# Optimization experiments

Hardware: AMD Instinct MI355X
Metric: run time of the kernel (lower is better)

The kernel has to match this reference:

```python
import jax, jax.numpy as jnp
import numpy as np

BLOCK = 512  # circulant block size

def block_circulant_matmul(x, w):
    """Block-circulant linear layer (CirCNN-style), no bias.
    x: (..., p*BLOCK); w: (q, p, BLOCK) -> out: (..., q*BLOCK).
    Each (q,p) block is a circulant matrix applied via FFT (circular conv).
    """
    q, p, b = w.shape
    xb = x.reshape(x.shape[:-1] + (p, b))            # (..., p, b)
    Xf = jnp.fft.rfft(xb, axis=-1)                    # (..., p, b//2+1) complex
    Wf = jnp.fft.rfft(w, axis=-1)                     # (q, p, b//2+1)
    Yf = jnp.einsum('...pf,qpf->...qf', Xf, Wf)       # sum over input blocks
    y = jnp.fft.irfft(Yf, n=b, axis=-1)               # (..., q, b)
    return y.reshape(x.shape[:-1] + (q * b,))

def setup_inputs() -> dict:
    key = jax.random.key(0)
    k1, k2, k3, k4 = jax.random.split(key, 4)
    d_model, d_ff, b = 2048, 5632, BLOCK
    p_in, q_ff = d_model // b, d_ff // b              # 4, 11
    scale = 1.0 / np.sqrt(d_model)
    x = jax.random.normal(k1, (4, 4096, d_model), dtype=jnp.float32)
    w_gate = jax.random.normal(k2, (q_ff, p_in, b), dtype=jnp.float32) * scale
    w_up   = jax.random.normal(k3, (q_ff, p_in, b), dtype=jnp.float32) * scale
    w_down = jax.random.normal(k4, (p_in, q_ff, b), dtype=jnp.float32) * (1.0 / np.sqrt(d_ff))
    return {"x": x, "w_gate": w_gate, "w_up": w_up, "w_down": w_down}

def reference(x, w_gate, w_up, w_down):
    # SwiGLU: down( SiLU(gate(x)) * up(x) ); dropout=0 -> identity
    gate = jax.nn.silu(block_circulant_matmul(x, w_gate))
    up = block_circulant_matmul(x, w_up)
    return block_circulant_matmul(gate * up, w_down)
```

## Files before the change

### kernel.cpp

```cpp
#include <hip/hip_runtime.h>
#include <math.h>


__device__ __forceinline__ int swz(int n) { return n ^ ((n >> 3) & 15); }

struct Tw { float t0r[7], t0i[7], t1r[7], t1i[7]; };

__device__ __forceinline__ void make_tw(int l, Tw& T)
{
    float c0, s0;
    __sincosf(-6.283185307179586f * (float)l * (1.0f/512.0f), &s0, &c0);
    float pr = c0, pi = s0;
    T.t0r[0] = pr; T.t0i[0] = pi;
#pragma unroll
    for (int m = 1; m < 7; ++m) {
        float nr = pr*c0 - pi*s0, ni = pr*s0 + pi*c0;
        pr = nr; pi = ni;
        T.t0r[m] = pr; T.t0i[m] = pi;
    }
    float c1, s1;
    __sincosf(-6.283185307179586f * (float)(l >> 3) * (1.0f/64.0f), &s1, &c1);
    pr = c1; pi = s1;
    T.t1r[0] = pr; T.t1i[0] = pi;
#pragma unroll
    for (int m = 1; m < 7; ++m) {
        float nr = pr*c1 - pi*s1, ni = pr*s1 + pi*c1;
        pr = nr; pi = ni;
        T.t1r[m] = pr; T.t1i[m] = pi;
    }
}

template<bool INV>
__device__ __forceinline__ void dft8(float xr[8], float xi[8])
{
    const float C = 0.70710678118654752f;
    float tr[4], ti[4], ur[4], ui[4];
#pragma unroll
    for (int q = 0; q < 4; ++q) {
        tr[q] = xr[q] + xr[q+4];  ti[q] = xi[q] + xi[q+4];
        ur[q] = xr[q] - xr[q+4];  ui[q] = xi[q] - xi[q+4];
    }
    {
        float xx = ur[1], yy = ui[1];
        if (!INV) { ur[1] = C*(xx+yy); ui[1] = C*(yy-xx); }
        else      { ur[1] = C*(xx-yy); ui[1] = C*(xx+yy); }
    }
    {
        float xx = ur[2], yy = ui[2];
        if (!INV) { ur[2] = yy;  ui[2] = -xx; }
        else      { ur[2] = -yy; ui[2] = xx; }
    }
    {
        float xx = ur[3], yy = ui[3];
        if (!INV) { ur[3] = C*(yy-xx);  ui[3] = -C*(xx+yy); }
        else      { ur[3] = -C*(xx+yy); ui[3] = C*(xx-yy); }
    }
    {
        float s0r=tr[0]+tr[2], s0i=ti[0]+ti[2];
        float d0r=tr[0]-tr[2], d0i=ti[0]-ti[2];
        float s1r=tr[1]+tr[3], s1i=ti[1]+ti[3];
        float e1r=tr[1]-tr[3], e1i=ti[1]-ti[3];
        float d1r, d1i;
        if (!INV) { d1r = e1i;  d1i = -e1r; } else { d1r = -e1i; d1i = e1r; }
        xr[0]=s0r+s1r; xi[0]=s0i+s1i;
        xr[2]=d0r+d1r; xi[2]=d0i+d1i;
        xr[4]=s0r-s1r; xi[4]=s0i-s1i;
        xr[6]=d0r-d1r; xi[6]=d0i-d1i;
    }
    {
        float s0r=ur[0]+ur[2], s0i=ui[0]+ui[2];
        float d0r=ur[0]-ur[2], d0i=ui[0]-ui[2];
        float s1r=ur[1]+ur[3], s1i=ui[1]+ui[3];
        float e1r=ur[1]-ur[3], e1i=ui[1]-ui[3];
        float d1r, d1i;
        if (!INV) { d1r = e1i;  d1i = -e1r; } else { d1r = -e1i; d1i = e1r; }
        xr[1]=s0r+s1r; xi[1]=s0i+s1i;
        xr[3]=d0r+d1r; xi[3]=d0i+d1i;
        xr[5]=s0r-s1r; xi[5]=s0i-s1i;
        xr[7]=d0r-d1r; xi[7]=d0i-d1i;
    }
}

template<bool INV>
__device__ __forceinline__ void twiddle7(float xr[8], float xi[8],
                                         const float* tr, const float* ti)
{
#pragma unroll
    for (int m = 1; m < 8; ++m) {
        float wr = tr[m-1], wi = INV ? -ti[m-1] : ti[m-1];
        float nr = xr[m]*wr - xi[m]*wi, ni = xr[m]*wi + xi[m]*wr;
        xr[m]=nr; xi[m]=ni;
    }
}

template<bool INV>
__device__ __forceinline__ void fft512_r8(float2* wk, int l, const Tw& T)
{
    float xr[8], xi[8];
#pragma unroll
    for (int q = 0; q < 8; ++q) { float2 v = wk[swz(l + 64*q)]; xr[q]=v.x; xi[q]=v.y; }
    dft8<INV>(xr, xi);
    twiddle7<INV>(xr, xi, T.t0r, T.t0i);
#pragma unroll
    for (int m = 0; m < 8; ++m) wk[swz(8*l + m)] = make_float2(xr[m], xi[m]);
#pragma unroll
    for (int q = 0; q < 8; ++q) { float2 v = wk[swz(l + 64*q)]; xr[q]=v.x; xi[q]=v.y; }
    dft8<INV>(xr, xi);
    twiddle7<INV>(xr, xi, T.t1r, T.t1i);
    {
        const int base = 64*(l>>3) + (l&7);
#pragma unroll
        for (int m = 0; m < 8; ++m) wk[swz(base + 8*m)] = make_float2(xr[m], xi[m]);
    }
#pragma unroll
    for (int q = 0; q < 8; ++q) { float2 v = wk[swz(l + 64*q)]; xr[q]=v.x; xi[q]=v.y; }
    dft8<INV>(xr, xi);
#pragma unroll
    for (int m = 0; m < 8; ++m) wk[swz(l + 64*m)] = make_float2(xr[m], xi[m]);
}

template<bool INV>
__device__ __forceinline__ void fft512_r8_head(float2* wk, int l, const Tw& T,
                                               float xr[8], float xi[8])
{
#pragma unroll
    for (int q = 0; q < 8; ++q) { float2 v = wk[swz(l + 64*q)]; xr[q]=v.x; xi[q]=v.y; }
    dft8<INV>(xr, xi);
    twiddle7<INV>(xr, xi, T.t0r, T.t0i);
#pragma unroll
    for (int m = 0; m < 8; ++m) wk[swz(8*l + m)] = make_float2(xr[m], xi[m]);
#pragma unroll
    for (int q = 0; q < 8; ++q) { float2 v = wk[swz(l + 64*q)]; xr[q]=v.x; xi[q]=v.y; }
    dft8<INV>(xr, xi);
    twiddle7<INV>(xr, xi, T.t1r, T.t1i);
    {
        const int base = 64*(l>>3) + (l&7);
#pragma unroll
        for (int m = 0; m < 8; ++m) wk[swz(base + 8*m)] = make_float2(xr[m], xi[m]);
    }
#pragma unroll
    for (int q = 0; q < 8; ++q) { float2 v = wk[swz(l + 64*q)]; xr[q]=v.x; xi[q]=v.y; }
    dft8<INV>(xr, xi);
}

template<bool INV>
__device__ __forceinline__ void fft512_r8_tail(float2* wk, int l, const Tw& T,
                                               float xr[8], float xi[8])
{
    dft8<INV>(xr, xi);
    twiddle7<INV>(xr, xi, T.t0r, T.t0i);
#pragma unroll
    for (int m = 0; m < 8; ++m) wk[swz(8*l + m)] = make_float2(xr[m], xi[m]);
#pragma unroll
    for (int q = 0; q < 8; ++q) { float2 v = wk[swz(l + 64*q)]; xr[q]=v.x; xi[q]=v.y; }
    dft8<INV>(xr, xi);
    twiddle7<INV>(xr, xi, T.t1r, T.t1i);
    {
        const int base = 64*(l>>3) + (l&7);
#pragma unroll
        for (int m = 0; m < 8; ++m) wk[swz(base + 8*m)] = make_float2(xr[m], xi[m]);
    }
#pragma unroll
    for (int q = 0; q < 8; ++q) { float2 v = wk[swz(l + 64*q)]; xr[q]=v.x; xi[q]=v.y; }
    dft8<INV>(xr, xi);
#pragma unroll
    for (int m = 0; m < 8; ++m) wk[swz(l + 64*m)] = make_float2(xr[m], xi[m]);
}

__global__ __launch_bounds__(64) void wf_prep(const float* __restrict__ wg,
                                              const float* __restrict__ wu,
                                              const float* __restrict__ wd,
                                              float2* __restrict__ wsp)
{
    __shared__ float2 wk[512];
    const int t = threadIdx.x;
    Tw T; make_tw(t, T);
    const int b = blockIdx.x;
    const float* src = (b < 44) ? (wg + (size_t)b * 512)
                     : (b < 88) ? (wu + (size_t)(b - 44) * 512)
                                : (wd + (size_t)(b - 88) * 512);
    float2* dst = wsp + (size_t)b * 257;

#pragma unroll
    for (int i = 0; i < 8; ++i) { int n = t + 64*i; wk[swz(n)] = make_float2(src[n], 0.f); }
    fft512_r8<false>(wk, t, T);
    const float sc = 1.0f / 512.0f;
#pragma unroll
    for (int i = 0; i < 5; ++i) {
        int k = t + 64*i;
        if (k <= 256) { float2 z = wk[swz(k)]; dst[k] = make_float2(sc*z.x, sc*z.y); }
    }
}

__global__ __launch_bounds__(256) void bcffn(const float* __restrict__ x,
                                             const float2* __restrict__ wsp,
                                             float* __restrict__ out)
{
    __shared__ float2 sWork[4 * 512];
    __shared__ float2 sXf[4][257];
    __shared__ float2 sHf[11][257];

    const int tid = threadIdx.x;
    const int t = tid & 63, w = tid >> 6;
    const size_t row = blockIdx.x;

    Tw T; make_tw(t, T);

    const float2* Wg = wsp;
    const float2* Wu = wsp + 44 * 257;
    const float2* Wd = wsp + 88 * 257;

    float2* wk = sWork + (w << 9);

    if (w < 2) {
        const float4* xa = (const float4*)(x + row * 2048 + (size_t)(2*w)   * 512);
        const float4* xb = (const float4*)(x + row * 2048 + (size_t)(2*w+1) * 512);
#pragma unroll
        for (int u = 0; u < 2; ++u) {
            int e = t + 64*u;
            float4 a = xa[e], b = xb[e];
            int n = 4*e;
            wk[swz(n+0)] = make_float2(a.x, b.x);
            wk[swz(n+1)] = make_float2(a.y, b.y);
            wk[swz(n+2)] = make_float2(a.z, b.z);
            wk[swz(n+3)] = make_float2(a.w, b.w);
        }
        fft512_r8<false>(wk, t, T);
#pragma unroll
        for (int u = 0; u < 5; ++u) {
            int k = t + 64*u;
            if (k <= 256) {
                float2 z = wk[swz(k)], m = wk[swz((512 - k) & 511)];
                sXf[2*w][k]   = make_float2(0.5f*(z.x + m.x), 0.5f*(z.y - m.y));
                sXf[2*w+1][k] = make_float2(0.5f*(z.y + m.y), 0.5f*(m.x - z.x));
            }
        }
    }
    __syncthreads();

    auto einsum_gu = [&](int q) {
#pragma unroll
        for (int u = 0; u < 5; ++u) {
            int k = t + 64*u;
            if (k <= 256) {
                float gr=0.f, gi=0.f, ur_=0.f, ui_=0.f;
#pragma unroll
                for (int p = 0; p < 4; ++p) {
                    float2 X = sXf[p][k];
                    float2 a = Wg[(q*4 + p)*257 + k];
                    float2 b = Wu[(q*4 + p)*257 + k];
                    gr  += X.x*a.x - X.y*a.y;  gi  += X.x*a.y + X.y*a.x;
                    ur_ += X.x*b.x - X.y*b.y;  ui_ += X.x*b.y + X.y*b.x;
                }
                wk[swz(k)] = make_float2(gr - ui_, gi + ur_);
                if (k != 0 && k != 256)
                    wk[swz(512 - k)] = make_float2(gr + ui_, ur_ - gi);
            }
        }
    };

    {
        const int qa = w, qb = w + 4;
        float har[8];
        float xr[8], xi[8];

        einsum_gu(qa);
        fft512_r8_head<true>(wk, t, T, xr, xi);
#pragma unroll
        for (int u = 0; u < 8; ++u)
            har[u] = xr[u] * xi[u] / (1.f + __expf(-xr[u]));

        einsum_gu(qb);
        fft512_r8_head<true>(wk, t, T, xr, xi);
#pragma unroll
        for (int u = 0; u < 8; ++u) {
            float hb = xr[u] * xi[u] / (1.f + __expf(-xr[u]));
            xr[u] = har[u];  xi[u] = hb;
        }
        fft512_r8_tail<false>(wk, t, T, xr, xi);
#pragma unroll
        for (int u = 0; u < 5; ++u) {
            int k = t + 64*u;
            if (k <= 256) {
                float2 z = wk[swz(k)], m = wk[swz((512 - k) & 511)];
                sHf[qa][k] = make_float2(0.5f*(z.x + m.x), 0.5f*(z.y - m.y));
                sHf[qb][k] = make_float2(0.5f*(z.y + m.y), 0.5f*(m.x - z.x));
            }
        }

        if (w < 3) {
            const int qc = w + 8;
            einsum_gu(qc);
            fft512_r8_head<true>(wk, t, T, xr, xi);
#pragma unroll
            for (int u = 0; u < 8; ++u) {
                xr[u] = xr[u] * xi[u] / (1.f + __expf(-xr[u]));
                xi[u] = 0.f;
            }
            fft512_r8_tail<false>(wk, t, T, xr, xi);
#pragma unroll
            for (int u = 0; u < 5; ++u) {
                int k = t + 64*u;
                if (k <= 256) sHf[qc][k] = wk[swz(k)];
            }
        }
    }
    __syncthreads();

    float Zr[5] = {0.f,0.f,0.f,0.f,0.f};
    float Zi[5] = {0.f,0.f,0.f,0.f,0.f};
#pragma unroll
    for (int u = 0; u < 5; ++u) {
        int k = t + 64*u;
        if (k <= 256) {
            float zr = 0.f, zi = 0.f;
#pragma unroll
            for (int q = 0; q < 11; ++q) {
                float2 H = sHf[q][k];
                float2 d = Wd[(w*11 + q)*257 + k];
                zr += H.x*d.x - H.y*d.y;
                zi += H.x*d.y + H.y*d.x;
            }
            Zr[u] = zr; Zi[u] = zi;
        }
    }
    if (w >= 2) {
#pragma unroll
        for (int u = 0; u < 5; ++u) {
            int k = t + 64*u;
            if (k <= 256) sXf[w-2][k] = make_float2(Zr[u], Zi[u]);
        }
    }
    __syncthreads();
    if (w < 2) {
#pragma unroll
        for (int u = 0; u < 5; ++u) {
            int k = t + 64*u;
            if (k <= 256) {
                float2 zb = sXf[w][k];
                wk[swz(k)] = make_float2(Zr[u] - zb.y, Zi[u] + zb.x);
                if (k != 0 && k != 256)
                    wk[swz(512 - k)] = make_float2(Zr[u] + zb.y, zb.x - Zi[u]);
            }
        }
        fft512_r8<true>(wk, t, T);
        float4* oa = (float4*)(out + row * 2048 + (size_t)w       * 512);
        float4* ob = (float4*)(out + row * 2048 + (size_t)(w + 2) * 512);
#pragma unroll
        for (int u = 0; u < 2; ++u) {
            int e = t + 64*u, n = 4*e;
            float2 v0 = wk[swz(n)],   v1 = wk[swz(n+1)];
            float2 v2 = wk[swz(n+2)], v3 = wk[swz(n+3)];
            oa[e] = make_float4(v0.x, v1.x, v2.x, v3.x);
            ob[e] = make_float4(v0.y, v1.y, v2.y, v3.y);
        }
    }
}

extern "C" void kernel_launch(void* const* d_in, const int* in_sizes, int n_in,
                              void* d_out, int out_size, void* d_ws, size_t ws_size,
                              hipStream_t stream)
{
    (void)n_in; (void)out_size; (void)ws_size;
    const float* x  = (const float*)d_in[0];
    const float* wg = (const float*)d_in[1];
    const float* wu = (const float*)d_in[2];
    const float* wd = (const float*)d_in[3];
    float2* wsp = (float2*)d_ws;
    float*  out = (float*)d_out;

    const int rows = in_sizes[0] / 2048;

    wf_prep<<<132, 64, 0, stream>>>(wg, wu, wd, wsp);
    bcffn<<<rows, 256, 0, stream>>>(x, wsp, out);
}
```

Before: 554.1 us.

## Process two rows per block with 8 waves and store spectra in half precision

Each block now handles two rows with 512 threads. Row pairs are packed into complex FFTs along the row dimension rather than the block dimension, so the down-projection combines directly in registers without an extra LDS exchange and barrier. The X and H spectra in LDS are stored as half2 to cut shared-memory footprint and traffic. Each down-weight load is reused for both rows. This adds fp16 rounding error on intermediate spectra and an uneven per-wave workload: 3 waves handle two q blocks, 5 waves handle one. It also assumes an even row count.

```diff
diff --git a/kernel.cpp b/kernel.cpp
--- a/kernel.cpp
+++ b/kernel.cpp
@@ -1,4 +1,5 @@
 #include <hip/hip_runtime.h>
+#include <hip/hip_fp16.h>
 #include <math.h>
 
 
@@ -192,17 +193,17 @@
     }
 }
 
-__global__ __launch_bounds__(256) void bcffn(const float* __restrict__ x,
+__global__ __launch_bounds__(512) void bcffn(const float* __restrict__ x,
                                              const float2* __restrict__ wsp,
                                              float* __restrict__ out)
 {
-    __shared__ float2 sWork[4 * 512];
-    __shared__ float2 sXf[4][257];
-    __shared__ float2 sHf[11][257];
+    __shared__ float2  sWork[8 * 512];
+    __shared__ __half2 sXf[2][4][257];
+    __shared__ __half2 sHf[2][11][257];
 
     const int tid = threadIdx.x;
     const int t = tid & 63, w = tid >> 6;
-    const size_t row = blockIdx.x;
+    const size_t row0 = (size_t)blockIdx.x * 2;
 
     Tw T; make_tw(t, T);
 
@@ -212,9 +213,10 @@
 
     float2* wk = sWork + (w << 9);
 
-    if (w < 2) {
-        const float4* xa = (const float4*)(x + row * 2048 + (size_t)(2*w)   * 512);
-        const float4* xb = (const float4*)(x + row * 2048 + (size_t)(2*w+1) * 512);
+    if (w >= 4) {
+        const int p = w - 4;
+        const float4* xa = (const float4*)(x + row0       * 2048 + (size_t)p * 512);
+        const float4* xb = (const float4*)(x + (row0 + 1) * 2048 + (size_t)p * 512);
 #pragma unroll
         for (int u = 0; u < 2; ++u) {
             int e = t + 64*u;
@@ -231,24 +233,24 @@
             int k = t + 64*u;
             if (k <= 256) {
                 float2 z = wk[swz(k)], m = wk[swz((512 - k) & 511)];
-                sXf[2*w][k]   = make_float2(0.5f*(z.x + m.x), 0.5f*(z.y - m.y));
-                sXf[2*w+1][k] = make_float2(0.5f*(z.y + m.y), 0.5f*(m.x - z.x));
+                sXf[0][p][k] = __floats2half2_rn(0.5f*(z.x + m.x), 0.5f*(z.y - m.y));
+                sXf[1][p][k] = __floats2half2_rn(0.5f*(z.y + m.y), 0.5f*(m.x - z.x));
             }
         }
     }
     __syncthreads();
 
-    auto einsum_gu = [&](int q) {
+    auto einsum_gu = [&](int q, int r) {
 #pragma unroll
         for (int u = 0; u < 5; ++u) {
             int k = t + 64*u;
             if (k <= 256) {
                 float gr=0.f, gi=0.f, ur_=0.f, ui_=0.f;
 #pragma unroll
-                for (int p = 0; p < 4; ++p) {
-                    float2 X = sXf[p][k];
-                    float2 a = Wg[(q*4 + p)*257 + k];
-                    float2 b = Wu[(q*4 + p)*257 + k];
+                for (int pp = 0; pp < 4; ++pp) {
+                    float2 X = __half22float2(sXf[r][pp][k]);
+                    float2 a = Wg[(q*4 + pp)*257 + k];
+                    float2 b = Wu[(q*4 + pp)*257 + k];
                     gr  += X.x*a.x - X.y*a.y;  gi  += X.x*a.y + X.y*a.x;
                     ur_ += X.x*b.x - X.y*b.y;  ui_ += X.x*b.y + X.y*b.x;
                 }
@@ -260,92 +262,70 @@
     };
 
     {
-        const int qa = w, qb = w + 4;
-        float har[8];
-        float xr[8], xi[8];
-
-        einsum_gu(qa);
-        fft512_r8_head<true>(wk, t, T, xr, xi);
-#pragma unroll
-        for (int u = 0; u < 8; ++u)
-            har[u] = xr[u] * xi[u] / (1.f + __expf(-xr[u]));
-
-        einsum_gu(qb);
-        fft512_r8_head<true>(wk, t, T, xr, xi);
-#pragma unroll
-        for (int u = 0; u < 8; ++u) {
-            float hb = xr[u] * xi[u] / (1.f + __expf(-xr[u]));
-            xr[u] = har[u];  xi[u] = hb;
-        }
-        fft512_r8_tail<false>(wk, t, T, xr, xi);
+        const int q0 = (w < 3) ? 2*w : w + 3;
+        const int nq = (w < 3) ? 2 : 1;
+        float har[8], xr[8], xi[8];
+#pragma unroll 1
+        for (int j = 0; j < nq; ++j) {
+            const int q = q0 + j;
+            einsum_gu(q, 0);
+            fft512_r8_head<true>(wk, t, T, xr, xi);
+#pragma unroll
+            for (int u = 0; u < 8; ++u)
+                har[u] = xr[u] * xi[u] * __frcp_rn(1.f + __expf(-xr[u]));
+            einsum_gu(q, 1);
+            fft512_r8_head<true>(wk, t, T, xr, xi);
+#pragma unroll
+            for (int u = 0; u < 8; ++u) {
+                float hb = xr[u] * xi[u] * __frcp_rn(1.f + __expf(-xr[u]));
+                xr[u] = har[u];  xi[u] = hb;
+            }
+            fft512_r8_tail<false>(wk, t, T, xr, xi);
+#pragma unroll
+            for (int u = 0; u < 5; ++u) {
+                int k = t + 64*u;
+                if (k <= 256) {
+                    float2 z = wk[swz(k)], m = wk[swz((512 - k) & 511)];
+                    sHf[0][q][k] = __floats2half2_rn(0.5f*(z.x + m.x), 0.5f*(z.y - m.y));
+                    sHf[1][q][k] = __floats2half2_rn(0.5f*(z.y + m.y), 0.5f*(m.x - z.x));
+                }
+            }
+        }
+    }
+    __syncthreads();
+
+    if (w >= 4) {
+        const int p = w - 4;
+        float Zr0[5]={0.f,0.f,0.f,0.f,0.f}, Zi0[5]={0.f,0.f,0.f,0.f,0.f};
+        float Zr1[5]={0.f,0.f,0.f,0.f,0.f}, Zi1[5]={0.f,0.f,0.f,0.f,0.f};
 #pragma unroll
         for (int u = 0; u < 5; ++u) {
             int k = t + 64*u;
             if (k <= 256) {
-                float2 z = wk[swz(k)], m = wk[swz((512 - k) & 511)];
-                sHf[qa][k] = make_float2(0.5f*(z.x + m.x), 0.5f*(z.y - m.y));
-                sHf[qb][k] = make_float2(0.5f*(z.y + m.y), 0.5f*(m.x - z.x));
-            }
-        }
-
-        if (w < 3) {
-            const int qc = w + 8;
-            einsum_gu(qc);
-            fft512_r8_head<true>(wk, t, T, xr, xi);
-#pragma unroll
-            for (int u = 0; u < 8; ++u) {
-                xr[u] = xr[u] * xi[u] / (1.f + __expf(-xr[u]));
-                xi[u] = 0.f;
-            }
-            fft512_r8_tail<false>(wk, t, T, xr, xi);
-#pragma unroll
-            for (int u = 0; u < 5; ++u) {
-                int k = t + 64*u;
-                if (k <= 256) sHf[qc][k] = wk[swz(k)];
-            }
-        }
-    }
-    __syncthreads();
-
-    float Zr[5] = {0.f,0.f,0.f,0.f,0.f};
-    float Zi[5] = {0.f,0.f,0.f,0.f,0.f};
-#pragma unroll
-    for (int u = 0; u < 5; ++u) {
-        int k = t + 64*u;
-        if (k <= 256) {
-            float zr = 0.f, zi = 0.f;
-#pragma unroll
-            for (int q = 0; q < 11; ++q) {
-                float2 H = sHf[q][k];
-                float2 d = Wd[(w*11 + q)*257 + k];
-                zr += H.x*d.x - H.y*d.y;
-                zi += H.x*d.y + H.y*d.x;
-            }
-            Zr[u] = zr; Zi[u] = zi;
-        }
-    }
-    if (w >= 2) {
-#pragma unroll
-        for (int u = 0; u < 5; ++u) {
-            int k = t + 64*u;
-            if (k <= 256) sXf[w-2][k] = make_float2(Zr[u], Zi[u]);
-        }
-    }
-    __syncthreads();
-    if (w < 2) {
+#pragma unroll
+                for (int q = 0; q < 11; ++q) {
+                    float2 d  = Wd[(p*11 + q)*257 + k];
+                    float2 H0 = __half22float2(sHf[0][q][k]);
+                    float2 H1 = __half22float2(sHf[1][q][k]);
+                    Zr0[u] += H0.x*d.x - H0.y*d.y;
+                    Zi0[u] += H0.x*d.y + H0.y*d.x;
+                    Zr1[u] += H1.x*d.x - H1.y*d.y;
+                    Zi1[u] += H1.x*d.y + H1.y*d.x;
+                }
+            }
+        }
 #pragma unroll
         for (int u = 0; u < 5; ++u) {
             int k = t + 64*u;
             if (k <= 256) {
-                float2 zb = sXf[w][k];
-                wk[swz(k)] = make_float2(Zr[u] - zb.y, Zi[u] + zb.x);
+                wk[swz(k)] = make_float2(Zr0[u] - Zi1[u], Zi0[u] + Zr1[u]);
                 if (k != 0 && k != 256)
-                    wk[swz(512 - k)] = make_float2(Zr[u] + zb.y, zb.x - Zi[u]);
+                    wk[swz(512 - k)] = make_float2(Zr0[u] + Zi1[u], Zr1[u] - Zi0[u]);
             }
         }
         fft512_r8<true>(wk, t, T);
-        float4* oa = (float4*)(out + row * 2048 + (size_t)w       * 512);
-        float4* ob = (float4*)(out + row * 2048 + (size_t)(w + 2) * 512);
+        float4* oa = (float4*)(out + row0       * 2048 + (size_t)p * 512);
+        float4* ob = (float4*)(out + (row0 + 1) * 2048 + (size_t)p * 512);
 #pragma unroll
         for (int u = 0; u < 2; ++u) {
             int e = t + 64*u, n = 4*e;
@@ -369,8 +349,9 @@
     float2* wsp = (float2*)d_ws;
     float*  out = (float*)d_out;
 
-    const int rows = in_sizes[0] / 2048;
+    const int rows   = in_sizes[0] / 2048;
+    const int blocks = rows / 2;
 
     wf_prep<<<132, 64, 0, stream>>>(wg, wu, wd, wsp);
-    bcffn<<<rows, 256, 0, stream>>>(x, wsp, out);
-}
+    bcffn<<<blocks, 512, 0, stream>>>(x, wsp, out);
+}
```

Result: slower. 574.2 us (+3.6%).
